# Performance work log

Hardware: AMD Instinct MI355X
Metric: run time of the kernel (lower is better)

## Reference

```python
import jax, jax.numpy as jnp
import numpy as np
import math

EPS = 1e-6
ROPE_BASE = 10000.0

def _rmsnorm(x, w):
    # normalize over last dim (head_dim)
    rms = jax.lax.rsqrt(jnp.mean(x * x, axis=-1, keepdims=True) + EPS)
    return x * rms * w

def _rope_cos_sin(seq_len, head_dim, dtype):
    inv_freq = 1.0 / (ROPE_BASE ** (jnp.arange(0, head_dim, 2, dtype=jnp.float32) / head_dim))
    t = jnp.arange(seq_len, dtype=jnp.float32)
    freqs = jnp.outer(t, inv_freq)            # [S, Dh/2]
    emb = jnp.concatenate([freqs, freqs], -1)  # [S, Dh]
    return jnp.cos(emb).astype(dtype), jnp.sin(emb).astype(dtype)

def _rotate_half(x):
    half = x.shape[-1] // 2
    return jnp.concatenate([-x[..., half:], x[..., :half]], axis=-1)

def setup_inputs() -> dict:
    key = jax.random.key(0)
    ks = jax.random.split(key, 6)
    B, S, E = 1, 2048, 2048
    H, KVH, Dh = 16, 4, 128
    x = jax.random.normal(ks[0], (B, S, E), dtype=jnp.float32)
    mask = jnp.triu(jnp.ones((S, S), dtype=bool), k=1)  # True = masked (causal)
    scale = 0.02
    Wq = jax.random.normal(ks[1], (E, E), dtype=jnp.float32) * scale
    Wk = jax.random.normal(ks[2], (KVH * Dh, E), dtype=jnp.float32) * scale
    Wv = jax.random.normal(ks[3], (KVH * Dh, E), dtype=jnp.float32) * scale
    Wo = jax.random.normal(ks[4], (E, E), dtype=jnp.float32) * scale
    q_norm_w = jnp.ones((Dh,), dtype=jnp.float32)
    k_norm_w = jnp.ones((Dh,), dtype=jnp.float32)
    return {"x": x, "mask": mask, "Wq": Wq, "Wk": Wk, "Wv": Wv, "Wo": Wo,
            "q_norm_w": q_norm_w, "k_norm_w": k_norm_w}

def reference(x, mask, Wq, Wk, Wv, Wo, q_norm_w, k_norm_w):
    B, S, E = x.shape
    H, Dh = 16, E // 16
    KVH = Wk.shape[0] // Dh
    rep = H // KVH
    # QKV projections (torch Linear: x @ W.T)
    q = (x @ Wq.T).reshape(B, S, H, Dh).transpose(0, 2, 1, 3)    # [B,H,S,Dh]
    k = (x @ Wk.T).reshape(B, S, KVH, Dh).transpose(0, 2, 1, 3)  # [B,KVH,S,Dh]
    v = (x @ Wv.T).reshape(B, S, KVH, Dh).transpose(0, 2, 1, 3)
    # QK-RMSNorm
    q = _rmsnorm(q, q_norm_w)
    k = _rmsnorm(k, k_norm_w)
    # RoPE
    cos, sin = _rope_cos_sin(S, Dh, q.dtype)  # [S,Dh]
    q = q * cos + _rotate_half(q) * sin
    k = k * cos + _rotate_half(k) * sin
    # GQA expand kv heads (repeat_interleave on head dim)
    k = jnp.repeat(k, rep, axis=1)  # [B,H,S,Dh]
    v = jnp.repeat(v, rep, axis=1)
    # SDPA (no yarn => scale = 1/sqrt(head_dim))
    scale = 1.0 / math.sqrt(Dh)
    scores = jnp.einsum('bhqd,bhkd->bhqk', q, k) * scale
    scores = jnp.where(mask[None, None, :, :], -jnp.inf, scores)
    attn = jax.nn.softmax(scores, axis=-1)
    attn = jnp.nan_to_num(attn, nan=0.0)
    out = jnp.einsum('bhqk,bhkd->bhqd', attn, v)
    out = out.transpose(0, 2, 1, 3).reshape(B, S, E)
    return out @ Wo.T
```

## Files before the change

kernel.cpp:

```cpp
#include <hip/hip_runtime.h>
#include <hip/hip_bf16.h>
#include <cstdint>
#include <cstddef>

using bf16 = __hip_bfloat16;
typedef __attribute__((ext_vector_type(8))) short short8;
typedef __attribute__((ext_vector_type(4))) float f32x4;

#define MFMA16(a, b, c) __builtin_amdgcn_mfma_f32_16x16x32_bf16((a), (b), (c), 0, 0, 0)

static constexpr int S = 2048;
static constexpr int E = 2048;
static constexpr int H = 16;
static constexpr int KVH = 4;
static constexpr int Dh = 128;
static constexpr int NQKV = 3072;
static constexpr float ATTN_SCALE = 0.08838834764831845f;

__device__ __forceinline__ short f2bs(float f) {
  __hip_bfloat16 h = __float2bfloat16(f);
  return *reinterpret_cast<short*>(&h);
}

__device__ __forceinline__ void gload_lds16(const void* g, void* l) {
  __builtin_amdgcn_global_load_lds(
      (const __attribute__((address_space(1))) unsigned int*)g,
      (__attribute__((address_space(3))) unsigned int*)l,
      16, 0, 0);
}

__global__ void cvt_bf16(const float* __restrict__ src, bf16* __restrict__ dst, int n) {
  int i = (blockIdx.x * 256 + threadIdx.x) * 8;
  if (i + 8 > n) return;
  const float4* s4 = reinterpret_cast<const float4*>(src + i);
  float4 a = s4[0];
  float4 b = s4[1];
  short8 o;
  o[0] = f2bs(a.x); o[1] = f2bs(a.y); o[2] = f2bs(a.z); o[3] = f2bs(a.w);
  o[4] = f2bs(b.x); o[5] = f2bs(b.y); o[6] = f2bs(b.z); o[7] = f2bs(b.w);
  *reinterpret_cast<short8*>(dst + i) = o;
}

template <bool OUT_F32>
__global__ __launch_bounds__(256, 2) void gemm_nt(const bf16* __restrict__ A,
                                                  const bf16* __restrict__ B,
                                                  void* __restrict__ Cout,
                                                  int M, int N, int K) {
  __shared__ bf16 As[128 * 32];
  __shared__ bf16 Bs[128 * 32];
  const int tid = threadIdx.x;
  const int lane = tid & 63;
  const int wv = tid >> 6;
  const int lr = lane & 15, lq = lane >> 4;
  const int wm = (wv >> 1) * 64, wn = (wv & 1) * 64;

  const int nwgx = M >> 7;
  const int nwg = (M >> 7) * (N >> 7);
  const int id = blockIdx.x + gridDim.x * blockIdx.y;
  const int sid = (id & 7) * (nwg >> 3) + (id >> 3);
  const int bm = (sid % nwgx) * 128, bn = (sid / nwgx) * 128;

  f32x4 acc[4][4] = {};

  for (int k0 = 0; k0 < K; k0 += 32) {
    __syncthreads();
    for (int it = 0; it < 2; ++it) {
      int ci = it * 256 + tid;
      int row = ci >> 2, co = (ci & 3) * 8;
      gload_lds16(A + (size_t)(bm + row) * K + k0 + co, As + (it * 256 + wv * 64) * 8);
      gload_lds16(B + (size_t)(bn + row) * K + k0 + co, Bs + (it * 256 + wv * 64) * 8);
    }
    __syncthreads();

    short8 af[4], bfr[4];
#pragma unroll
    for (int im = 0; im < 4; ++im)
      af[im] = *reinterpret_cast<const short8*>(As + (wm + im * 16 + lr) * 32 + lq * 8);
#pragma unroll
    for (int jn = 0; jn < 4; ++jn)
      bfr[jn] = *reinterpret_cast<const short8*>(Bs + (wn + jn * 16 + lr) * 32 + lq * 8);
#pragma unroll
    for (int im = 0; im < 4; ++im)
#pragma unroll
      for (int jn = 0; jn < 4; ++jn)
        acc[im][jn] = MFMA16(af[im], bfr[jn], acc[im][jn]);
  }

#pragma unroll
  for (int im = 0; im < 4; ++im)
#pragma unroll
    for (int jn = 0; jn < 4; ++jn)
#pragma unroll
      for (int i = 0; i < 4; ++i) {
        int r = bm + wm + im * 16 + lq * 4 + i;
        int c = bn + wn + jn * 16 + lr;
        if (OUT_F32)
          reinterpret_cast<float*>(Cout)[(size_t)r * N + c] = acc[im][jn][i];
        else
          reinterpret_cast<bf16*>(Cout)[(size_t)r * N + c] = __float2bfloat16(acc[im][jn][i]);
      }
}

__global__ __launch_bounds__(256, 2) void gemm_nt64(const bf16* __restrict__ A,
                                                    const bf16* __restrict__ B,
                                                    float* __restrict__ Cout,
                                                    int M, int N, int K) {
  __shared__ bf16 As[128 * 32];
  __shared__ bf16 Bs[64 * 32];
  const int tid = threadIdx.x;
  const int lane = tid & 63;
  const int wv = tid >> 6;
  const int lr = lane & 15, lq = lane >> 4;
  const int wm = (wv >> 1) * 64, wn = (wv & 1) * 32;

  const int nwgx = M >> 7;
  const int nwg = (M >> 7) * (N >> 6);
  const int id = blockIdx.x + gridDim.x * blockIdx.y;
  const int sid = (id & 7) * (nwg >> 3) + (id >> 3);
  const int bm = (sid % nwgx) * 128, bn = (sid / nwgx) * 64;

  f32x4 acc[4][2] = {};

  for (int k0 = 0; k0 < K; k0 += 32) {
    __syncthreads();
#pragma unroll
    for (int it = 0; it < 2; ++it) {
      int ci = it * 256 + tid;
      int row = ci >> 2, co = (ci & 3) * 8;
      gload_lds16(A + (size_t)(bm + row) * K + k0 + co, As + (it * 256 + wv * 64) * 8);
    }
    {
      int ci = tid;
      int row = ci >> 2, co = (ci & 3) * 8;
      gload_lds16(B + (size_t)(bn + row) * K + k0 + co, Bs + (wv * 64) * 8);
    }
    __syncthreads();

    short8 af[4], bfr[2];
#pragma unroll
    for (int im = 0; im < 4; ++im)
      af[im] = *reinterpret_cast<const short8*>(As + (wm + im * 16 + lr) * 32 + lq * 8);
#pragma unroll
    for (int jn = 0; jn < 2; ++jn)
      bfr[jn] = *reinterpret_cast<const short8*>(Bs + (wn + jn * 16 + lr) * 32 + lq * 8);
#pragma unroll
    for (int im = 0; im < 4; ++im)
#pragma unroll
      for (int jn = 0; jn < 2; ++jn)
        acc[im][jn] = MFMA16(af[im], bfr[jn], acc[im][jn]);
  }

#pragma unroll
  for (int im = 0; im < 4; ++im)
#pragma unroll
    for (int jn = 0; jn < 2; ++jn)
#pragma unroll
      for (int i = 0; i < 4; ++i) {
        int r = bm + wm + im * 16 + lq * 4 + i;
        int c = bn + wn + jn * 16 + lr;
        Cout[(size_t)r * N + c] = acc[im][jn][i];
      }
}

__global__ void qk_norm_rope(const bf16* __restrict__ QKV,
                             const float* __restrict__ qw, const float* __restrict__ kw,
                             bf16* __restrict__ Qn, bf16* __restrict__ Kn) {
  const int lane = threadIdx.x & 63;
  const int w = threadIdx.x >> 6;
  const int row = blockIdx.x * 4 + w;
  const int s = row / 20;
  const int hh = row % 20;

  const bf16* src;
  bf16* dst;
  const float* wt;
  float outscale;
  if (hh < 16) {
    src = QKV + (size_t)s * NQKV + hh * Dh;
    dst = Qn + ((size_t)hh * S + s) * Dh;
    wt = qw;
    outscale = ATTN_SCALE;
  } else {
    int kvh = hh - 16;
    src = QKV + (size_t)s * NQKV + 2048 + kvh * Dh;
    dst = Kn + ((size_t)kvh * S + s) * Dh;
    wt = kw;
    outscale = 1.0f;
  }

  float x0 = __bfloat162float(src[lane]);
  float x1 = __bfloat162float(src[lane + 64]);
  float ss = x0 * x0 + x1 * x1;
#pragma unroll
  for (int off = 1; off < 64; off <<= 1) ss += __shfl_xor(ss, off);
  float rms = rsqrtf(ss * (1.0f / 128.0f) + 1e-6f);
  float n0 = x0 * rms * wt[lane];
  float n1 = x1 * rms * wt[lane + 64];

  float inv_freq = exp2f((float)lane * -0.2076205059304601f);
  float ang = (float)s * inv_freq;
  float sn, cs;
  sincosf(ang, &sn, &cs);
  float o0 = (n0 * cs - n1 * sn) * outscale;
  float o1 = (n1 * cs + n0 * sn) * outscale;
  dst[lane] = __float2bfloat16(o0);
  dst[lane + 64] = __float2bfloat16(o1);
}

__global__ void v_transpose(const bf16* __restrict__ QKV, bf16* __restrict__ Vt) {
  __shared__ bf16 t[64][65];
  const int s0 = blockIdx.x * 64;
  const int c0 = blockIdx.y * 64;
  const int kvh = c0 >> 7, d0 = c0 & 127;
#pragma unroll 4
  for (int i = 0; i < 16; ++i) {
    int lin = i * 256 + threadIdx.x;
    int r = lin >> 6, c = lin & 63;
    t[r][c] = QKV[(size_t)(s0 + r) * NQKV + 2560 + c0 + c];
  }
  __syncthreads();
#pragma unroll 4
  for (int i = 0; i < 16; ++i) {
    int lin = i * 256 + threadIdx.x;
    int d = lin >> 6, s = lin & 63;
    Vt[((size_t)kvh * 128 + d0 + d) * S + s0 + s] = t[s][d];
  }
}

__device__ __forceinline__ void chunk_decode(int u, int& qi, int& c, int& nc) {
  if (u < 8)       { qi = u;               c = 0;      nc = 1; }
  else if (u < 24) { int v = u - 8;  qi = 8  + (v >> 1); c = v & 1;  nc = 2; }
  else if (u < 48) { int v = u - 24; qi = 16 + v / 3;    c = v % 3;  nc = 3; }
  else             { int v = u - 48; qi = 24 + (v >> 2); c = v & 3;  nc = 4; }
}

__global__ __launch_bounds__(256, 2) void attn_fwd(const bf16* __restrict__ Qn,
                                                   const bf16* __restrict__ Kn,
                                                   const bf16* __restrict__ Vt,
                                                   bf16* __restrict__ AO,
                                                   bf16* __restrict__ Opart,
                                                   float* __restrict__ ml) {
  __shared__ bf16 Ks[2][64 * 128];
  __shared__ bf16 Vs[2][128 * 64];
  __shared__ bf16 Ps[4][16 * 64];

  const int tid = threadIdx.x;
  const int lane = tid & 63;
  const int w = tid >> 6;
  const int lr = lane & 15, lq = lane >> 4;

  const int bx = blockIdx.x;
  const int h = bx / 80, u = bx % 80;
  int qi, cch, nc;
  chunk_decode(u, qi, cch, nc);
  const int kvh = h >> 2;
  const int q0 = qi * 64;
  const int t0 = cch * 8;
  const int t1 = min(t0 + 8, qi + 1);

  const bf16* Qbase = Qn + ((size_t)h * S + q0 + w * 16) * Dh;
  const bf16* Kbase = Kn + (size_t)kvh * S * Dh;
  const bf16* Vbase = Vt + (size_t)kvh * Dh * S;
  bf16* Pw = &Ps[w][0];

  short8 qf[4];
#pragma unroll
  for (int dd = 0; dd < 4; ++dd)
    qf[dd] = *reinterpret_cast<const short8*>(Qbase + (size_t)lr * Dh + dd * 32 + lq * 8);

  short8 ones;
#pragma unroll
  for (int e = 0; e < 8; ++e) ones[e] = (short)0x3F80;

  float mrow[4];
  f32x4 lacc = {};
  f32x4 oacc[8] = {};
#pragma unroll
  for (int i = 0; i < 4; ++i) mrow[i] = -INFINITY;

  auto stageK = [&](int tile, int b) {
    const int kb = tile * 64;
#pragma unroll
    for (int i = 0; i < 4; ++i) {
      int chunk = i * 256 + tid;
      int r = chunk >> 4, c = chunk & 15;
      int cs = c ^ (r & 7);
      gload_lds16(Kbase + (size_t)(kb + r) * Dh + cs * 8,
                  (bf16*)Ks + b * 8192 + (i * 256 + w * 64) * 8);
    }
  };
  auto stageV = [&](int tile, int b) {
    const int kb = tile * 64;
#pragma unroll
    for (int i = 0; i < 4; ++i) {
      int chunk = i * 256 + tid;
      int r = chunk >> 3, c = chunk & 7;
      int cs = c ^ (r & 7);
      gload_lds16(Vbase + (size_t)r * S + kb + cs * 8,
                  (bf16*)Vs + b * 8192 + (i * 256 + w * 64) * 8);
    }
  };

  stageK(t0, 0);
  stageV(t0, 0);
  __syncthreads();
  int buf = 0;

  for (int t = t0; t < t1; ++t) {
    if (t + 1 < t1) { stageK(t + 1, buf ^ 1); stageV(t + 1, buf ^ 1); }

    f32x4 sacc[4] = {};
    __builtin_amdgcn_s_setprio(1);
#pragma unroll
    for (int jn = 0; jn < 4; ++jn) {
      int r = jn * 16 + lr;
      const char* kroww = (const char*)Ks + buf * 16384 + r * 256;
      int rx = r & 7;
#pragma unroll
      for (int dd = 0; dd < 4; ++dd) {
        int cg = (dd * 4 + lq) ^ rx;
        short8 bfr = *reinterpret_cast<const short8*>(kroww + cg * 16);
        sacc[jn] = MFMA16(qf[dd], bfr, sacc[jn]);
      }
    }
    __builtin_amdgcn_s_setprio(0);

    const bool diag = (t == qi);
    float pm[4] = {-INFINITY, -INFINITY, -INFINITY, -INFINITY};
#pragma unroll
    for (int jn = 0; jn < 4; ++jn)
#pragma unroll
      for (int i = 0; i < 4; ++i) {
        float v = sacc[jn][i];
        if (diag && (jn * 16 + lr > w * 16 + lq * 4 + i)) v = -INFINITY;
        sacc[jn][i] = v;
        pm[i] = fmaxf(pm[i], v);
      }
#pragma unroll
    for (int i = 0; i < 4; ++i) {
      pm[i] = fmaxf(pm[i], __shfl_xor(pm[i], 1));
      pm[i] = fmaxf(pm[i], __shfl_xor(pm[i], 2));
      pm[i] = fmaxf(pm[i], __shfl_xor(pm[i], 4));
      pm[i] = fmaxf(pm[i], __shfl_xor(pm[i], 8));
    }
    float dm = fmaxf(fmaxf(pm[0] - mrow[0], pm[1] - mrow[1]),
                     fmaxf(pm[2] - mrow[2], pm[3] - mrow[3]));
    if (!__all(dm <= 8.0f)) {
#pragma unroll
      for (int i = 0; i < 4; ++i) {
        float mnew = fmaxf(mrow[i], pm[i]);
        float a = __expf(mrow[i] - mnew);
        mrow[i] = mnew;
        lacc[i] *= a;
#pragma unroll
        for (int jd = 0; jd < 8; ++jd) oacc[jd][i] *= a;
      }
    }
#pragma unroll
    for (int jn = 0; jn < 4; ++jn)
#pragma unroll
      for (int i = 0; i < 4; ++i) {
        float p = __expf(sacc[jn][i] - mrow[i]);
        int row = lq * 4 + i;
        int col = jn * 16 + lr;
        int swz = ((col >> 3) ^ (row & 7));
        Pw[row * 64 + swz * 8 + (col & 7)] = __float2bfloat16(p);
      }

    __builtin_amdgcn_wave_barrier();

    __builtin_amdgcn_s_setprio(1);
#pragma unroll
    for (int kk = 0; kk < 2; ++kk) {
      int swz = (kk * 4 + lq) ^ (lr & 7);
      short8 pa = *reinterpret_cast<const short8*>(Pw + lr * 64 + swz * 8);
      lacc = MFMA16(pa, ones, lacc);
#pragma unroll
      for (int jd = 0; jd < 8; ++jd) {
        int r = jd * 16 + lr;
        int cg = (kk * 4 + lq) ^ (r & 7);
        short8 vf = *reinterpret_cast<const short8*>((const char*)Vs + buf * 16384 + r * 128 + cg * 16);
        oacc[jd] = MFMA16(pa, vf, oacc[jd]);
      }
    }
    __builtin_amdgcn_s_setprio(0);

    __syncthreads();
    buf ^= 1;
  }

  if (nc == 1) {
#pragma unroll
    for (int jd = 0; jd < 8; ++jd)
#pragma unroll
      for (int i = 0; i < 4; ++i) {
        float o = oacc[jd][i] / lacc[i];
        AO[(size_t)(q0 + w * 16 + lq * 4 + i) * E + h * Dh + jd * 16 + lr] = __float2bfloat16(o);
      }
  } else {
    const int pidx = h * 80 + u;
    bf16* Op = Opart + (size_t)pidx * 64 * 128;
#pragma unroll
    for (int jd = 0; jd < 8; ++jd)
#pragma unroll
      for (int i = 0; i < 4; ++i)
        Op[(w * 16 + lq * 4 + i) * 128 + jd * 16 + lr] = __float2bfloat16(oacc[jd][i]);
    if (lr == 0) {
#pragma unroll
      for (int i = 0; i < 4; ++i) {
        int row = w * 16 + lq * 4 + i;
        ml[(size_t)pidx * 128 + row * 2]     = mrow[i];
        ml[(size_t)pidx * 128 + row * 2 + 1] = lacc[i];
      }
    }
  }
}

__global__ __launch_bounds__(256) void attn_combine(const bf16* __restrict__ Opart,
                                                    const float* __restrict__ ml,
                                                    bf16* __restrict__ AO) {
  const int qi = 8 + blockIdx.x;
  const int h = blockIdx.y;
  const int nc = qi / 8 + 1;
  const int off = (qi < 16) ? 8 + (qi - 8) * 2
                : (qi < 24) ? 24 + (qi - 16) * 3
                            : 48 + (qi - 24) * 4;
  const int base = h * 80 + off;
  const int row = threadIdx.x >> 2;
  const int d0 = (threadIdx.x & 3) * 32;

  float mc[4], lc[4];
  float M = -INFINITY;
  for (int c = 0; c < nc; ++c) {
    mc[c] = ml[(size_t)(base + c) * 128 + row * 2];
    lc[c] = ml[(size_t)(base + c) * 128 + row * 2 + 1];
    M = fmaxf(M, mc[c]);
  }
  float L = 0.0f;
  float acc[32];
#pragma unroll
  for (int j = 0; j < 32; ++j) acc[j] = 0.0f;
  for (int c = 0; c < nc; ++c) {
    float wgt = __expf(mc[c] - M);
    L += wgt * lc[c];
    const short8* op = reinterpret_cast<const short8*>(
        Opart + (size_t)(base + c) * 8192 + row * 128 + d0);
#pragma unroll
    for (int j4 = 0; j4 < 4; ++j4) {
      short8 vv = op[j4];
#pragma unroll
      for (int e = 0; e < 8; ++e) {
        short sv = vv[e];
        acc[j4 * 8 + e] += wgt * __bfloat162float(*reinterpret_cast<bf16*>(&sv));
      }
    }
  }
  float inv = 1.0f / L;
  bf16* ao = AO + (size_t)(qi * 64 + row) * E + h * Dh + d0;
  short8 outv[4];
#pragma unroll
  for (int j4 = 0; j4 < 4; ++j4) {
#pragma unroll
    for (int e = 0; e < 8; ++e) outv[j4][e] = f2bs(acc[j4 * 8 + e] * inv);
    reinterpret_cast<short8*>(ao)[j4] = outv[j4];
  }
}

extern "C" void kernel_launch(void* const* d_in, const int* in_sizes, int n_in,
                              void* d_out, int out_size, void* d_ws, size_t ws_size,
                              hipStream_t stream) {
  const float* x  = (const float*)d_in[0];
  const float* Wq = (const float*)d_in[2];
  const float* Wk = (const float*)d_in[3];
  const float* Wv = (const float*)d_in[4];
  const float* Wo = (const float*)d_in[5];
  const float* qw = (const float*)d_in[6];
  const float* kw = (const float*)d_in[7];

  char* ws = (char*)d_ws;
  bf16* xb   = (bf16*)(ws + (0ull << 20));
  bf16* Wcat = (bf16*)(ws + (8ull << 20));
  bf16* Wob  = (bf16*)(ws + (20ull << 20));
  bf16* QKV  = (bf16*)(ws + (28ull << 20));
  bf16* Qn   = (bf16*)(ws + (40ull << 20));
  bf16* Kn   = (bf16*)(ws + (48ull << 20));
  bf16* Vt   = (bf16*)(ws + (50ull << 20));
  bf16* AO   = (bf16*)(ws + (52ull << 20));
  bf16* Opart = (bf16*)(ws + (0ull << 20));
  float* ml   = (float*)(ws + (28ull << 20));

  cvt_bf16<<<2048, 256, 0, stream>>>(x, xb, E * S);
  cvt_bf16<<<2048, 256, 0, stream>>>(Wq, Wcat, E * E);
  cvt_bf16<<<512, 256, 0, stream>>>(Wk, Wcat + 2048 * 2048, 512 * E);
  cvt_bf16<<<512, 256, 0, stream>>>(Wv, Wcat + 2560 * 2048, 512 * E);
  cvt_bf16<<<2048, 256, 0, stream>>>(Wo, Wob, E * E);

  gemm_nt<false><<<dim3(S / 128, NQKV / 128), 256, 0, stream>>>(xb, Wcat, QKV, S, NQKV, E);

  qk_norm_rope<<<(S * 20) / 4, 256, 0, stream>>>(QKV, qw, kw, Qn, Kn);
  v_transpose<<<dim3(S / 64, 512 / 64), 256, 0, stream>>>(QKV, Vt);

  attn_fwd<<<16 * 80, 256, 0, stream>>>(Qn, Kn, Vt, AO, Opart, ml);
  attn_combine<<<dim3(24, 16), 256, 0, stream>>>(Opart, ml, AO);

  gemm_nt64<<<dim3(S / 128, E / 64), 256, 0, stream>>>(AO, Wob, (float*)d_out, S, E, E);
}
```

Measured before the change: 178.1 us.

## Compute transposed scores and pass P through registers instead of LDS

Swaps the MFMA operands in the QK^T step so each lane holds the scores of a single query row. This lets the row max be reduced with two cross-lane shuffles and a single running max per lane. The probability tile is packed into bf16 pairs and rearranged into the PV A-operand layout with lane shuffles, which removes the per-wave LDS staging buffer and its wave barrier. In exchange it adds many shuffle and select instructions, plus broadcasting the rescale factor back to the accumulator layout.

```diff
diff --git a/kernel.cpp b/kernel.cpp
--- a/kernel.cpp
+++ b/kernel.cpp
@@ -6,6 +6,7 @@
 using bf16 = __hip_bfloat16;
 typedef __attribute__((ext_vector_type(8))) short short8;
 typedef __attribute__((ext_vector_type(4))) float f32x4;
+typedef __attribute__((ext_vector_type(4))) unsigned int u32x4;
 
 #define MFMA16(a, b, c) __builtin_amdgcn_mfma_f32_16x16x32_bf16((a), (b), (c), 0, 0, 0)
 
@@ -16,10 +17,16 @@
 static constexpr int Dh = 128;
 static constexpr int NQKV = 3072;
 static constexpr float ATTN_SCALE = 0.08838834764831845f;
+static constexpr float NEG_BIG = -1e30f;
 
 __device__ __forceinline__ short f2bs(float f) {
   __hip_bfloat16 h = __float2bfloat16(f);
   return *reinterpret_cast<short*>(&h);
+}
+
+__device__ __forceinline__ unsigned int pack_bf16(float lo, float hi) {
+  return ((unsigned int)(unsigned short)f2bs(hi) << 16) |
+         (unsigned int)(unsigned short)f2bs(lo);
 }
 
 __device__ __forceinline__ void gload_lds16(const void* g, void* l) {
@@ -242,7 +249,6 @@
                                                    float* __restrict__ ml) {
   __shared__ bf16 Ks[2][64 * 128];
   __shared__ bf16 Vs[2][128 * 64];
-  __shared__ bf16 Ps[4][16 * 64];
 
   const int tid = threadIdx.x;
   const int lane = tid & 63;
@@ -261,7 +267,6 @@
   const bf16* Qbase = Qn + ((size_t)h * S + q0 + w * 16) * Dh;
   const bf16* Kbase = Kn + (size_t)kvh * S * Dh;
   const bf16* Vbase = Vt + (size_t)kvh * Dh * S;
-  bf16* Pw = &Ps[w][0];
 
   short8 qf[4];
 #pragma unroll
@@ -272,11 +277,9 @@
 #pragma unroll
   for (int e = 0; e < 8; ++e) ones[e] = (short)0x3F80;
 
-  float mrow[4];
+  float m = NEG_BIG;
   f32x4 lacc = {};
   f32x4 oacc[8] = {};
-#pragma unroll
-  for (int i = 0; i < 4; ++i) mrow[i] = -INFINITY;
 
   auto stageK = [&](int tile, int b) {
     const int kb = tile * 64;
@@ -319,68 +322,76 @@
 #pragma unroll
       for (int dd = 0; dd < 4; ++dd) {
         int cg = (dd * 4 + lq) ^ rx;
-        short8 bfr = *reinterpret_cast<const short8*>(kroww + cg * 16);
-        sacc[jn] = MFMA16(qf[dd], bfr, sacc[jn]);
+        short8 kf = *reinterpret_cast<const short8*>(kroww + cg * 16);
+        sacc[jn] = MFMA16(kf, qf[dd], sacc[jn]);
       }
     }
     __builtin_amdgcn_s_setprio(0);
 
     const bool diag = (t == qi);
-    float pm[4] = {-INFINITY, -INFINITY, -INFINITY, -INFINITY};
+    float p[4][4];
+    float pm = NEG_BIG;
 #pragma unroll
     for (int jn = 0; jn < 4; ++jn)
 #pragma unroll
       for (int i = 0; i < 4; ++i) {
         float v = sacc[jn][i];
-        if (diag && (jn * 16 + lr > w * 16 + lq * 4 + i)) v = -INFINITY;
-        sacc[jn][i] = v;
-        pm[i] = fmaxf(pm[i], v);
-      }
-#pragma unroll
-    for (int i = 0; i < 4; ++i) {
-      pm[i] = fmaxf(pm[i], __shfl_xor(pm[i], 1));
-      pm[i] = fmaxf(pm[i], __shfl_xor(pm[i], 2));
-      pm[i] = fmaxf(pm[i], __shfl_xor(pm[i], 4));
-      pm[i] = fmaxf(pm[i], __shfl_xor(pm[i], 8));
-    }
-    float dm = fmaxf(fmaxf(pm[0] - mrow[0], pm[1] - mrow[1]),
-                     fmaxf(pm[2] - mrow[2], pm[3] - mrow[3]));
-    if (!__all(dm <= 8.0f)) {
+        if (diag && (jn * 16 + lq * 4 + i > w * 16 + lr)) v = NEG_BIG;
+        p[jn][i] = v;
+        pm = fmaxf(pm, v);
+      }
+    pm = fmaxf(pm, __shfl_xor(pm, 16));
+    pm = fmaxf(pm, __shfl_xor(pm, 32));
+
+    if (!__all(pm - m <= 8.0f)) {
+      float mnew = fmaxf(m, pm);
+      float a = __expf(m - mnew);
+      m = mnew;
+      float aq[4];
+#pragma unroll
+      for (int i = 0; i < 4; ++i) aq[i] = __shfl(a, lq * 4 + i);
 #pragma unroll
       for (int i = 0; i < 4; ++i) {
-        float mnew = fmaxf(mrow[i], pm[i]);
-        float a = __expf(mrow[i] - mnew);
-        mrow[i] = mnew;
-        lacc[i] *= a;
-#pragma unroll
-        for (int jd = 0; jd < 8; ++jd) oacc[jd][i] *= a;
-      }
-    }
+        lacc[i] *= aq[i];
+#pragma unroll
+        for (int jd = 0; jd < 8; ++jd) oacc[jd][i] *= aq[i];
+      }
+    }
+
+    unsigned int wd[4][2];
 #pragma unroll
     for (int jn = 0; jn < 4; ++jn)
 #pragma unroll
-      for (int i = 0; i < 4; ++i) {
-        float p = __expf(sacc[jn][i] - mrow[i]);
-        int row = lq * 4 + i;
-        int col = jn * 16 + lr;
-        int swz = ((col >> 3) ^ (row & 7));
-        Pw[row * 64 + swz * 8 + (col & 7)] = __float2bfloat16(p);
-      }
-
-    __builtin_amdgcn_wave_barrier();
+      for (int uu = 0; uu < 2; ++uu) {
+        float plo = __expf(p[jn][2 * uu] - m);
+        float phi = __expf(p[jn][2 * uu + 1] - m);
+        wd[jn][uu] = pack_bf16(plo, phi);
+      }
+
+    short8 pa[2];
+#pragma unroll
+    for (int kk = 0; kk < 2; ++kk) {
+      u32x4 w4;
+#pragma unroll
+      for (int tt = 0; tt < 4; ++tt) {
+        int sl = lr + 16 * ((lq & 1) * 2 + (tt >> 1));
+        unsigned int s0 = __shfl(wd[kk * 2][tt & 1], sl);
+        unsigned int s1 = __shfl(wd[kk * 2 + 1][tt & 1], sl);
+        w4[tt] = (lq >> 1) ? s1 : s0;
+      }
+      pa[kk] = __builtin_bit_cast(short8, w4);
+    }
 
     __builtin_amdgcn_s_setprio(1);
 #pragma unroll
     for (int kk = 0; kk < 2; ++kk) {
-      int swz = (kk * 4 + lq) ^ (lr & 7);
-      short8 pa = *reinterpret_cast<const short8*>(Pw + lr * 64 + swz * 8);
-      lacc = MFMA16(pa, ones, lacc);
+      lacc = MFMA16(pa[kk], ones, lacc);
 #pragma unroll
       for (int jd = 0; jd < 8; ++jd) {
         int r = jd * 16 + lr;
         int cg = (kk * 4 + lq) ^ (r & 7);
         short8 vf = *reinterpret_cast<const short8*>((const char*)Vs + buf * 16384 + r * 128 + cg * 16);
-        oacc[jd] = MFMA16(pa, vf, oacc[jd]);
+        oacc[jd] = MFMA16(pa[kk], vf, oacc[jd]);
       }
     }
     __builtin_amdgcn_s_setprio(0);
@@ -405,13 +416,12 @@
 #pragma unroll
       for (int i = 0; i < 4; ++i)
         Op[(w * 16 + lq * 4 + i) * 128 + jd * 16 + lr] = __float2bfloat16(oacc[jd][i]);
+    if (lq == 0)
+      ml[(size_t)pidx * 128 + (w * 16 + lr) * 2] = m;
     if (lr == 0) {
 #pragma unroll
-      for (int i = 0; i < 4; ++i) {
-        int row = w * 16 + lq * 4 + i;
-        ml[(size_t)pidx * 128 + row * 2]     = mrow[i];
-        ml[(size_t)pidx * 128 + row * 2 + 1] = lacc[i];
-      }
+      for (int i = 0; i < 4; ++i)
+        ml[(size_t)pidx * 128 + (w * 16 + lq * 4 + i) * 2 + 1] = lacc[i];
     }
   }
 }
```

After: 174.8 us. No clear change (-1.8%).
